# Performance work log

Hardware: AMD Instinct MI355X
Metric: run time of the kernel (lower is better)

The kernel has to match this reference:

```python
import jax, jax.numpy as jnp
import numpy as np

DEPTH = 512      # hidden width of each Linear (arg name 'depth' in the torch code)
WIDTH = 8        # number of hidden blocks (arg name 'width')
IN_DIM = 4       # x_dim=3 + is_unsteady=1
OUT_DIM = 4
N = 32768


def _mlp(x, W0, b0, Wh, bh, Wf, bf):
    # Faithful to torch Sequential: Linear, then (width-1) x [Linear, Tanh], then Linear.
    # Note: NO tanh after the very first Linear (matches the original module).
    h = x @ W0 + b0                      # [N, DEPTH]
    for i in range(Wh.shape[0]):         # width-1 hidden blocks (small fixed loop)
        h = jnp.tanh(h @ Wh[i] + bh[i])
    return h @ Wf + bf                   # [N, 4]


def setup_inputs() -> dict:
    key = jax.random.key(0)
    ks = jax.random.split(key, 8)
    s_in = 1.0 / np.sqrt(IN_DIM)
    s_h = 1.0 / np.sqrt(DEPTH)
    return {
        "x": jax.random.normal(ks[0], (N, IN_DIM), dtype=jnp.float32),
        "W0": jax.random.uniform(ks[1], (IN_DIM, DEPTH), jnp.float32, -s_in, s_in),
        "b0": jax.random.uniform(ks[2], (DEPTH,), jnp.float32, -s_in, s_in),
        "Wh": jax.random.uniform(ks[3], (WIDTH - 1, DEPTH, DEPTH), jnp.float32, -s_h, s_h),
        "bh": jax.random.uniform(ks[4], (WIDTH - 1, DEPTH), jnp.float32, -s_h, s_h),
        "Wf": jax.random.uniform(ks[5], (DEPTH, OUT_DIM), jnp.float32, -s_h, s_h),
        "bf": jax.random.uniform(ks[6], (OUT_DIM,), jnp.float32, -s_h, s_h),
    }


def reference(x, W0, b0, Wh, bh, Wf, bf):
    # a = MLP(x); then 4 batched VJPs w.r.t. x with cotangents e_0..e_3
    # (exactly what the torch curl() does with autograd.grad).
    a, vjp = jax.vjp(lambda xx: _mlp(xx, W0, b0, Wh, bh, Wf, bf), x)
    e = jnp.eye(OUT_DIM, dtype=a.dtype)
    da0 = vjp(jnp.broadcast_to(e[0], a.shape))[0]   # [N, 4] = d a_0 / d x
    da1 = vjp(jnp.broadcast_to(e[1], a.shape))[0]
    da2 = vjp(jnp.broadcast_to(e[2], a.shape))[0]
    dp  = vjp(jnp.broadcast_to(e[3], a.shape))[0]
    u = jnp.stack([
        da2[:, 1] - da1[:, 2],
        da0[:, 2] - da2[:, 0],
        da1[:, 0] - da0[:, 1],
        dp[:, 0], dp[:, 1], dp[:, 2],
    ], axis=1)                                       # [N, 6]
    return u
```

## Files before the change

kernel.cpp:

```cpp
#include <hip/hip_runtime.h>
#include <stdint.h>

typedef short bf16x8 __attribute__((ext_vector_type(8)));
typedef float f32x4  __attribute__((ext_vector_type(4)));
typedef uint32_t u32;

#define NSAMP  32768
#define D      512
#define RPB    16
#define NLAYER 7
#define KSN    16
#define WL_U32 131072

union U4B { uint4 u; u32 w[4]; bf16x8 s; };
__device__ __forceinline__ bf16x8 as_frag(uint4 v) { U4B c; c.u = v; return c.s; }

__device__ __forceinline__ u32 bfr(float f) {
    u32 b = __float_as_uint(f);
    return (b + 0x7fffu + ((b >> 16) & 1u)) >> 16;
}
__device__ __forceinline__ float bf2f(u32 h) { return __uint_as_float(h << 16); }
__device__ __forceinline__ u32 packpair(float v) {
    u32 h = bfr(v);
    u32 l = bfr(v - bf2f(h));
    return h | (l << 16);
}
__device__ __forceinline__ float fast_tanh(float z) {
    const float e = __expf(2.f * z);
    return 1.f - 2.f / (e + 1.f);
}

__global__ void pack_weights(const float* __restrict__ Wh,
                             u32* __restrict__ whi, u32* __restrict__ wlo) {
    const int L    = blockIdx.x >> 4;
    const int ks   = blockIdx.x & 15;
    const int lane = threadIdx.x & 63;
    const int half = threadIdx.x >> 6;
    const float* src = Wh + (size_t)L * D * D + (size_t)(ks * 32 + half * 8) * D;
    for (int nb = 0; nb < D; nb += 64) {
        const int n = nb + lane;
        float v[8];
        #pragma unroll
        for (int i = 0; i < 8; ++i) v[i] = src[(size_t)i * D + n];
        u32 hi[4], lo[4];
        #pragma unroll
        for (int j = 0; j < 4; ++j) {
            u32 h0 = bfr(v[2*j]),   l0 = bfr(v[2*j]   - bf2f(h0));
            u32 h1 = bfr(v[2*j+1]), l1 = bfr(v[2*j+1] - bf2f(h1));
            hi[j] = h0 | (h1 << 16);
            lo[j] = l0 | (l1 << 16);
        }
        const size_t idx4 = (size_t)((L * 16 + ks) * 512 + n) * 4 + half;
        *(uint4*)(whi + idx4 * 4) = *(uint4*)hi;
        *(uint4*)(wlo + idx4 * 4) = *(uint4*)lo;
    }
}

__global__ __launch_bounds__(1024)
void mlp_curl_mfma(const float* __restrict__ x,
                   const float* __restrict__ W0,
                   const float* __restrict__ b0,
                   const float* __restrict__ bhid,
                   const float* __restrict__ Wf,
                   const u32* __restrict__ whi,
                   const u32* __restrict__ wlo,
                   float* __restrict__ out)
{
    __shared__ uint4 AHi[4096];
    __shared__ uint4 ALo[1024];

    const int t    = threadIdx.x;
    const int g    = t >> 6, lane = t & 63;
    const int lrow = lane & 15, lq = lane >> 4;
    const int cg   = g;
    const int n0   = blockIdx.x * RPB;

    {
        const int R  = g >> 2, c4 = g & 3;
        const float4 xv = *(const float4*)(x + (size_t)(n0 + lrow) * 4);
        #pragma unroll
        for (int ksl = 0; ksl < 4; ++ksl) {
            const int ks = c4 * 4 + ksl;
            const int c0 = ks * 32 + lq * 8;
            float v[8];
            if (R == 0) {
                #pragma unroll
                for (int j = 0; j < 8; ++j)
                    v[j] = b0[c0 + j]
                         + xv.x * W0[c0 + j]         + xv.y * W0[D + c0 + j]
                         + xv.z * W0[2 * D + c0 + j] + xv.w * W0[3 * D + c0 + j];
                u32 pp[8];
                #pragma unroll
                for (int j = 0; j < 8; ++j) pp[j] = packpair(v[j]);
                uint4 hi, lo;
                hi.x = (pp[0] & 0xffffu) | (pp[1] << 16);  lo.x = (pp[0] >> 16) | (pp[1] & 0xffff0000u);
                hi.y = (pp[2] & 0xffffu) | (pp[3] << 16);  lo.y = (pp[2] >> 16) | (pp[3] & 0xffff0000u);
                hi.z = (pp[4] & 0xffffu) | (pp[5] << 16);  lo.z = (pp[4] >> 16) | (pp[5] & 0xffff0000u);
                hi.w = (pp[6] & 0xffffu) | (pp[7] << 16);  lo.w = (pp[6] >> 16) | (pp[7] & 0xffff0000u);
                AHi[ks * 64 + lane] = hi;
                ALo[ks * 64 + lane] = lo;
            } else {
                const float* wr = W0 + (size_t)(R - 1) * D;
                #pragma unroll
                for (int j = 0; j < 8; ++j) v[j] = wr[c0 + j];
                uint4 hi;
                hi.x = bfr(v[0]) | (bfr(v[1]) << 16);
                hi.y = bfr(v[2]) | (bfr(v[3]) << 16);
                hi.z = bfr(v[4]) | (bfr(v[5]) << 16);
                hi.w = bfr(v[6]) | (bfr(v[7]) << 16);
                AHi[(R * 16 + ks) * 64 + lane] = hi;
            }
        }
    }
    __syncthreads();

    const u32 boff0 = ((u32)(cg * 32 + lrow) * 4 + lq) * 4;
    const u32 boff1 = boff0 + 256;

    for (int L = 0; L < NLAYER; ++L) {
        const u32* __restrict__ whiL = whi + (size_t)L * WL_U32;
        const u32* __restrict__ wloL = wlo + (size_t)L * WL_U32;
        f32x4 acc[4][2];
        #pragma unroll
        for (int R = 0; R < 4; ++R) { acc[R][0] = (f32x4)0.f; acc[R][1] = (f32x4)0.f; }

        #pragma unroll 2
        for (int ks = 0; ks < KSN; ++ks) {
            const size_t off = (size_t)ks * 8192;
            const uint4 Bh0 = *(const uint4*)(whiL + off + boff0);
            const uint4 Bh1 = *(const uint4*)(whiL + off + boff1);
            const uint4 Bl0 = *(const uint4*)(wloL + off + boff0);
            const uint4 Bl1 = *(const uint4*)(wloL + off + boff1);
            {
                const bf16x8 a_hi = as_frag(AHi[ks * 64 + lane]);
                const bf16x8 a_lo = as_frag(ALo[ks * 64 + lane]);
                const bf16x8 b0h = as_frag(Bh0), b0l = as_frag(Bl0);
                const bf16x8 b1h = as_frag(Bh1), b1l = as_frag(Bl1);
                acc[0][0] = __builtin_amdgcn_mfma_f32_16x16x32_bf16(a_lo, b0h, acc[0][0], 0, 0, 0);
                acc[0][0] = __builtin_amdgcn_mfma_f32_16x16x32_bf16(a_hi, b0l, acc[0][0], 0, 0, 0);
                acc[0][0] = __builtin_amdgcn_mfma_f32_16x16x32_bf16(a_hi, b0h, acc[0][0], 0, 0, 0);
                acc[0][1] = __builtin_amdgcn_mfma_f32_16x16x32_bf16(a_lo, b1h, acc[0][1], 0, 0, 0);
                acc[0][1] = __builtin_amdgcn_mfma_f32_16x16x32_bf16(a_hi, b1l, acc[0][1], 0, 0, 0);
                acc[0][1] = __builtin_amdgcn_mfma_f32_16x16x32_bf16(a_hi, b1h, acc[0][1], 0, 0, 0);
            }
            #pragma unroll
            for (int R = 1; R < 4; ++R) {
                const bf16x8 a_hi = as_frag(AHi[(R * 16 + ks) * 64 + lane]);
                const bf16x8 b0h = as_frag(Bh0), b0l = as_frag(Bl0);
                const bf16x8 b1h = as_frag(Bh1), b1l = as_frag(Bl1);
                acc[R][0] = __builtin_amdgcn_mfma_f32_16x16x32_bf16(a_hi, b0l, acc[R][0], 0, 0, 0);
                acc[R][0] = __builtin_amdgcn_mfma_f32_16x16x32_bf16(a_hi, b0h, acc[R][0], 0, 0, 0);
                acc[R][1] = __builtin_amdgcn_mfma_f32_16x16x32_bf16(a_hi, b1l, acc[R][1], 0, 0, 0);
                acc[R][1] = __builtin_amdgcn_mfma_f32_16x16x32_bf16(a_hi, b1h, acc[R][1], 0, 0, 0);
            }
        }
        __syncthreads();

        float tp[2][4];
        #pragma unroll
        for (int ct = 0; ct < 2; ++ct) {
            const int col = cg * 32 + ct * 16 + lrow;
            const float bias = bhid[(size_t)L * D + col];
            const int k = ct * 16 + lrow;
            #pragma unroll
            for (int q = 0; q < 4; ++q) {
                const float h = fast_tanh(acc[0][ct][q] + bias);
                tp[ct][q] = (1.f - h) * (1.f + h);
                if (L < NLAYER - 1) {
                    const u32 pp = packpair(h);
                    const u32 byte = ((u32)((cg * 64) + (k >> 3) * 16 + (lq * 4 + q)) << 4)
                                   | ((u32)(k & 7) << 1);
                    *(uint16_t*)((char*)AHi + byte) = (uint16_t)(pp & 0xffffu);
                    *(uint16_t*)((char*)ALo + byte) = (uint16_t)(pp >> 16);
                }
            }
        }

        if (L < NLAYER - 1) {
            #pragma unroll
            for (int R = 1; R < 4; ++R)
                #pragma unroll
                for (int ct = 0; ct < 2; ++ct) {
                    const int k = ct * 16 + lrow;
                    #pragma unroll
                    for (int q = 0; q < 4; ++q) {
                        const u32 hb = bfr(acc[R][ct][q] * tp[ct][q]);
                        const u32 byte = ((u32)(((R * 16 + cg) * 64) + (k >> 3) * 16 + (lq * 4 + q)) << 4)
                                       | ((u32)(k & 7) << 1);
                        *(uint16_t*)((char*)AHi + byte) = (uint16_t)hb;
                    }
                }
        } else {
            #pragma unroll
            for (int i = 0; i < 3; ++i) {
                float Jrow[4][4];
                #pragma unroll
                for (int q = 0; q < 4; ++q)
                    #pragma unroll
                    for (int o = 0; o < 4; ++o) Jrow[q][o] = 0.f;
                #pragma unroll
                for (int ct = 0; ct < 2; ++ct) {
                    const int col = cg * 32 + ct * 16 + lrow;
                    const float4 wf = *(const float4*)(Wf + (size_t)col * 4);
                    #pragma unroll
                    for (int q = 0; q < 4; ++q) {
                        const float jv = acc[i + 1][ct][q] * tp[ct][q];
                        Jrow[q][0] += jv * wf.x;
                        Jrow[q][1] += jv * wf.y;
                        Jrow[q][2] += jv * wf.z;
                        Jrow[q][3] += jv * wf.w;
                    }
                }
                #pragma unroll
                for (int m = 1; m <= 8; m <<= 1)
                    #pragma unroll
                    for (int q = 0; q < 4; ++q)
                        #pragma unroll
                        for (int o = 0; o < 4; ++o)
                            Jrow[q][o] += __shfl_xor(Jrow[q][o], m);
                if (lrow == 0) {
                    float* JT = (float*)AHi;
                    #pragma unroll
                    for (int q = 0; q < 4; ++q) {
                        const int s = lq * 4 + q;
                        #pragma unroll
                        for (int o = 0; o < 4; ++o)
                            JT[((cg * 3 + i) * 16 + s) * 4 + o] = Jrow[q][o];
                    }
                }
            }
        }
        __syncthreads();
    }

    if (t < RPB * 6) {
        const float* JT = (const float*)AHi;
        const int s = t / 6, c = t % 6;
        float J[3][4];
        #pragma unroll
        for (int i = 0; i < 3; ++i)
            #pragma unroll
            for (int o = 0; o < 4; ++o) {
                float v = 0.f;
                for (int w = 0; w < 16; ++w) v += JT[((w * 3 + i) * 16 + s) * 4 + o];
                J[i][o] = v;
            }
        float v;
        if      (c == 0) v = J[1][2] - J[2][1];
        else if (c == 1) v = J[2][0] - J[0][2];
        else if (c == 2) v = J[0][1] - J[1][0];
        else if (c == 3) v = J[0][3];
        else if (c == 4) v = J[1][3];
        else             v = J[2][3];
        out[(size_t)(n0 + s) * 6 + c] = v;
    }
}

extern "C" void kernel_launch(void* const* d_in, const int* in_sizes, int n_in,
                              void* d_out, int out_size, void* d_ws, size_t ws_size,
                              hipStream_t stream) {
    const float* x  = (const float*)d_in[0];
    const float* W0 = (const float*)d_in[1];
    const float* b0 = (const float*)d_in[2];
    const float* Wh = (const float*)d_in[3];
    const float* bh = (const float*)d_in[4];
    const float* Wf = (const float*)d_in[5];
    u32* whi = (u32*)d_ws;
    u32* wlo = whi + (size_t)NLAYER * WL_U32;
    pack_weights<<<NLAYER * 16, 256, 0, stream>>>(Wh, whi, wlo);
    mlp_curl_mfma<<<NSAMP / RPB, 1024, 0, stream>>>(x, W0, b0, bh, Wf, whi, wlo, (float*)d_out);
}
```

Measured before the change: 1.112 ms.

## Pack primal and tangent rows into two MFMA tiles with eight samples per block

Each block now handles 8 samples instead of 16. The forward activations and the three tangent streams are packed into two 16-row MFMA tiles: rows 0-7 of the first tile hold the primal and rows 8-15 hold the first tangent. Each of 8 warps covers 64 output columns, and the block size is halved to 512 threads with a launch-bounds occupancy hint, so shared memory per block shrinks. The aim is better occupancy and fewer wasted tangent tiles. In exchange, each sample re-reads more weight data from L2, and the hi/lo split-precision MFMA is now also applied to the first tangent rows, which adds MFMA work.

```diff
diff --git a/kernel.cpp b/kernel.cpp
--- a/kernel.cpp
+++ b/kernel.cpp
@@ -7,7 +7,7 @@
 
 #define NSAMP  32768
 #define D      512
-#define RPB    16
+#define RPB    8
 #define NLAYER 7
 #define KSN    16
 #define WL_U32 131072
@@ -56,7 +56,7 @@
     }
 }
 
-__global__ __launch_bounds__(1024)
+__global__ __launch_bounds__(512, 4)
 void mlp_curl_mfma(const float* __restrict__ x,
                    const float* __restrict__ W0,
                    const float* __restrict__ b0,
@@ -66,149 +66,131 @@
                    const u32* __restrict__ wlo,
                    float* __restrict__ out)
 {
-    __shared__ uint4 AHi[4096];
+    __shared__ uint4 AHi[2048];
     __shared__ uint4 ALo[1024];
+    __shared__ float JT[768];
 
     const int t    = threadIdx.x;
     const int g    = t >> 6, lane = t & 63;
     const int lrow = lane & 15, lq = lane >> 4;
-    const int cg   = g;
+    const int c0   = g * 64;
     const int n0   = blockIdx.x * RPB;
 
     {
-        const int R  = g >> 2, c4 = g & 3;
-        const float4 xv = *(const float4*)(x + (size_t)(n0 + lrow) * 4);
-        #pragma unroll
-        for (int ksl = 0; ksl < 4; ++ksl) {
-            const int ks = c4 * 4 + ksl;
-            const int c0 = ks * 32 + lq * 8;
-            float v[8];
-            if (R == 0) {
-                #pragma unroll
-                for (int j = 0; j < 8; ++j)
-                    v[j] = b0[c0 + j]
-                         + xv.x * W0[c0 + j]         + xv.y * W0[D + c0 + j]
-                         + xv.z * W0[2 * D + c0 + j] + xv.w * W0[3 * D + c0 + j];
-                u32 pp[8];
-                #pragma unroll
-                for (int j = 0; j < 8; ++j) pp[j] = packpair(v[j]);
-                uint4 hi, lo;
-                hi.x = (pp[0] & 0xffffu) | (pp[1] << 16);  lo.x = (pp[0] >> 16) | (pp[1] & 0xffff0000u);
-                hi.y = (pp[2] & 0xffffu) | (pp[3] << 16);  lo.y = (pp[2] >> 16) | (pp[3] & 0xffff0000u);
-                hi.z = (pp[4] & 0xffffu) | (pp[5] << 16);  lo.z = (pp[4] >> 16) | (pp[5] & 0xffff0000u);
-                hi.w = (pp[6] & 0xffffu) | (pp[7] << 16);  lo.w = (pp[6] >> 16) | (pp[7] & 0xffff0000u);
-                AHi[ks * 64 + lane] = hi;
-                ALo[ks * 64 + lane] = lo;
-            } else {
-                const float* wr = W0 + (size_t)(R - 1) * D;
-                #pragma unroll
-                for (int j = 0; j < 8; ++j) v[j] = wr[c0 + j];
-                uint4 hi;
-                hi.x = bfr(v[0]) | (bfr(v[1]) << 16);
-                hi.y = bfr(v[2]) | (bfr(v[3]) << 16);
-                hi.z = bfr(v[4]) | (bfr(v[5]) << 16);
-                hi.w = bfr(v[6]) | (bfr(v[7]) << 16);
-                AHi[(R * 16 + ks) * 64 + lane] = hi;
-            }
+        const int r = lrow;
+        const float4 xv = *(const float4*)(x + (size_t)(n0 + (r & 7)) * 4);
+        #pragma unroll
+        for (int ksl = 0; ksl < 2; ++ksl) {
+            const int ks = g * 2 + ksl;
+            const int cb = ks * 32 + lq * 8;
+            float v0[8], v1[8];
+            #pragma unroll
+            for (int j = 0; j < 8; ++j) {
+                const int c = cb + j;
+                const float w0 = W0[c], w1 = W0[D + c], w2 = W0[2*D + c], w3 = W0[3*D + c];
+                v0[j] = (r < 8) ? (b0[c] + xv.x*w0 + xv.y*w1 + xv.z*w2 + xv.w*w3) : w0;
+                v1[j] = (r < 8) ? w1 : w2;
+            }
+            u32 pp[8];
+            #pragma unroll
+            for (int j = 0; j < 8; ++j) pp[j] = packpair(v0[j]);
+            uint4 hi, lo;
+            hi.x = (pp[0] & 0xffffu) | (pp[1] << 16);  lo.x = (pp[0] >> 16) | (pp[1] & 0xffff0000u);
+            hi.y = (pp[2] & 0xffffu) | (pp[3] << 16);  lo.y = (pp[2] >> 16) | (pp[3] & 0xffff0000u);
+            hi.z = (pp[4] & 0xffffu) | (pp[5] << 16);  lo.z = (pp[4] >> 16) | (pp[5] & 0xffff0000u);
+            hi.w = (pp[6] & 0xffffu) | (pp[7] << 16);  lo.w = (pp[6] >> 16) | (pp[7] & 0xffff0000u);
+            AHi[ks * 64 + lane] = hi;
+            ALo[ks * 64 + lane] = lo;
+            uint4 h1;
+            h1.x = bfr(v1[0]) | (bfr(v1[1]) << 16);
+            h1.y = bfr(v1[2]) | (bfr(v1[3]) << 16);
+            h1.z = bfr(v1[4]) | (bfr(v1[5]) << 16);
+            h1.w = bfr(v1[6]) | (bfr(v1[7]) << 16);
+            AHi[(16 + ks) * 64 + lane] = h1;
         }
     }
     __syncthreads();
 
-    const u32 boff0 = ((u32)(cg * 32 + lrow) * 4 + lq) * 4;
-    const u32 boff1 = boff0 + 256;
+    u32 boff[4];
+    #pragma unroll
+    for (int ct = 0; ct < 4; ++ct)
+        boff[ct] = ((u32)(c0 + ct * 16 + lrow) * 4 + (u32)lq) * 4;
 
     for (int L = 0; L < NLAYER; ++L) {
         const u32* __restrict__ whiL = whi + (size_t)L * WL_U32;
         const u32* __restrict__ wloL = wlo + (size_t)L * WL_U32;
-        f32x4 acc[4][2];
-        #pragma unroll
-        for (int R = 0; R < 4; ++R) { acc[R][0] = (f32x4)0.f; acc[R][1] = (f32x4)0.f; }
+        f32x4 acc[2][4];
+        #pragma unroll
+        for (int ct = 0; ct < 4; ++ct) { acc[0][ct] = (f32x4)0.f; acc[1][ct] = (f32x4)0.f; }
 
         #pragma unroll 2
         for (int ks = 0; ks < KSN; ++ks) {
+            const bf16x8 a0h = as_frag(AHi[ks * 64 + lane]);
+            const bf16x8 a0l = as_frag(ALo[ks * 64 + lane]);
+            const bf16x8 a1h = as_frag(AHi[(16 + ks) * 64 + lane]);
             const size_t off = (size_t)ks * 8192;
-            const uint4 Bh0 = *(const uint4*)(whiL + off + boff0);
-            const uint4 Bh1 = *(const uint4*)(whiL + off + boff1);
-            const uint4 Bl0 = *(const uint4*)(wloL + off + boff0);
-            const uint4 Bl1 = *(const uint4*)(wloL + off + boff1);
-            {
-                const bf16x8 a_hi = as_frag(AHi[ks * 64 + lane]);
-                const bf16x8 a_lo = as_frag(ALo[ks * 64 + lane]);
-                const bf16x8 b0h = as_frag(Bh0), b0l = as_frag(Bl0);
-                const bf16x8 b1h = as_frag(Bh1), b1l = as_frag(Bl1);
-                acc[0][0] = __builtin_amdgcn_mfma_f32_16x16x32_bf16(a_lo, b0h, acc[0][0], 0, 0, 0);
-                acc[0][0] = __builtin_amdgcn_mfma_f32_16x16x32_bf16(a_hi, b0l, acc[0][0], 0, 0, 0);
-                acc[0][0] = __builtin_amdgcn_mfma_f32_16x16x32_bf16(a_hi, b0h, acc[0][0], 0, 0, 0);
-                acc[0][1] = __builtin_amdgcn_mfma_f32_16x16x32_bf16(a_lo, b1h, acc[0][1], 0, 0, 0);
-                acc[0][1] = __builtin_amdgcn_mfma_f32_16x16x32_bf16(a_hi, b1l, acc[0][1], 0, 0, 0);
-                acc[0][1] = __builtin_amdgcn_mfma_f32_16x16x32_bf16(a_hi, b1h, acc[0][1], 0, 0, 0);
-            }
-            #pragma unroll
-            for (int R = 1; R < 4; ++R) {
-                const bf16x8 a_hi = as_frag(AHi[(R * 16 + ks) * 64 + lane]);
-                const bf16x8 b0h = as_frag(Bh0), b0l = as_frag(Bl0);
-                const bf16x8 b1h = as_frag(Bh1), b1l = as_frag(Bl1);
-                acc[R][0] = __builtin_amdgcn_mfma_f32_16x16x32_bf16(a_hi, b0l, acc[R][0], 0, 0, 0);
-                acc[R][0] = __builtin_amdgcn_mfma_f32_16x16x32_bf16(a_hi, b0h, acc[R][0], 0, 0, 0);
-                acc[R][1] = __builtin_amdgcn_mfma_f32_16x16x32_bf16(a_hi, b1l, acc[R][1], 0, 0, 0);
-                acc[R][1] = __builtin_amdgcn_mfma_f32_16x16x32_bf16(a_hi, b1h, acc[R][1], 0, 0, 0);
+            #pragma unroll
+            for (int ct = 0; ct < 4; ++ct) {
+                const bf16x8 bh = as_frag(*(const uint4*)(whiL + off + boff[ct]));
+                const bf16x8 bl = as_frag(*(const uint4*)(wloL + off + boff[ct]));
+                acc[0][ct] = __builtin_amdgcn_mfma_f32_16x16x32_bf16(a0l, bh, acc[0][ct], 0, 0, 0);
+                acc[0][ct] = __builtin_amdgcn_mfma_f32_16x16x32_bf16(a0h, bl, acc[0][ct], 0, 0, 0);
+                acc[0][ct] = __builtin_amdgcn_mfma_f32_16x16x32_bf16(a0h, bh, acc[0][ct], 0, 0, 0);
+                acc[1][ct] = __builtin_amdgcn_mfma_f32_16x16x32_bf16(a1h, bl, acc[1][ct], 0, 0, 0);
+                acc[1][ct] = __builtin_amdgcn_mfma_f32_16x16x32_bf16(a1h, bh, acc[1][ct], 0, 0, 0);
             }
         }
         __syncthreads();
 
-        float tp[2][4];
-        #pragma unroll
-        for (int ct = 0; ct < 2; ++ct) {
-            const int col = cg * 32 + ct * 16 + lrow;
+        float tpv[4][4];
+        #pragma unroll
+        for (int ct = 0; ct < 4; ++ct) {
+            const int col  = c0 + ct * 16 + lrow;
             const float bias = bhid[(size_t)L * D + col];
-            const int k = ct * 16 + lrow;
+            const int ks_s = g * 2 + (ct >> 1);
+            const int k_in = (ct & 1) * 16 + lrow;
             #pragma unroll
             for (int q = 0; q < 4; ++q) {
-                const float h = fast_tanh(acc[0][ct][q] + bias);
-                tp[ct][q] = (1.f - h) * (1.f + h);
+                const float z0 = acc[0][ct][q];
+                const float h  = fast_tanh(z0 + bias);
+                const float tv = __shfl((1.f - h) * (1.f + h), lane & 31);
+                tpv[ct][q] = tv;
                 if (L < NLAYER - 1) {
-                    const u32 pp = packpair(h);
-                    const u32 byte = ((u32)((cg * 64) + (k >> 3) * 16 + (lq * 4 + q)) << 4)
-                                   | ((u32)(k & 7) << 1);
-                    *(uint16_t*)((char*)AHi + byte) = (uint16_t)(pp & 0xffffu);
-                    *(uint16_t*)((char*)ALo + byte) = (uint16_t)(pp >> 16);
+                    const float v0 = (lane < 32) ? h : z0 * tv;
+                    const u32 pp = packpair(v0);
+                    const u32 fl = (u32)(((k_in >> 3) * 16) + lq * 4 + q);
+                    const u32 b0b = ((u32)(ks_s * 64) + fl) * 16 + ((u32)(k_in & 7) << 1);
+                    *(uint16_t*)((char*)AHi + b0b) = (uint16_t)(pp & 0xffffu);
+                    *(uint16_t*)((char*)ALo + b0b) = (uint16_t)(pp >> 16);
+                    const float v1 = acc[1][ct][q] * tv;
+                    const u32 b1b = ((u32)((16 + ks_s) * 64) + fl) * 16 + ((u32)(k_in & 7) << 1);
+                    *(uint16_t*)((char*)AHi + b1b) = (uint16_t)bfr(v1);
                 }
             }
         }
 
-        if (L < NLAYER - 1) {
-            #pragma unroll
-            for (int R = 1; R < 4; ++R)
-                #pragma unroll
-                for (int ct = 0; ct < 2; ++ct) {
-                    const int k = ct * 16 + lrow;
-                    #pragma unroll
-                    for (int q = 0; q < 4; ++q) {
-                        const u32 hb = bfr(acc[R][ct][q] * tp[ct][q]);
-                        const u32 byte = ((u32)(((R * 16 + cg) * 64) + (k >> 3) * 16 + (lq * 4 + q)) << 4)
-                                       | ((u32)(k & 7) << 1);
-                        *(uint16_t*)((char*)AHi + byte) = (uint16_t)hb;
-                    }
-                }
-        } else {
+        if (L == NLAYER - 1) {
             #pragma unroll
             for (int i = 0; i < 3; ++i) {
-                float Jrow[4][4];
+                float Jr[4][4];
                 #pragma unroll
                 for (int q = 0; q < 4; ++q)
                     #pragma unroll
-                    for (int o = 0; o < 4; ++o) Jrow[q][o] = 0.f;
+                    for (int o = 0; o < 4; ++o) Jr[q][o] = 0.f;
                 #pragma unroll
-                for (int ct = 0; ct < 2; ++ct) {
-                    const int col = cg * 32 + ct * 16 + lrow;
+                for (int ct = 0; ct < 4; ++ct) {
+                    const int col = c0 + ct * 16 + lrow;
                     const float4 wf = *(const float4*)(Wf + (size_t)col * 4);
                     #pragma unroll
                     for (int q = 0; q < 4; ++q) {
-                        const float jv = acc[i + 1][ct][q] * tp[ct][q];
-                        Jrow[q][0] += jv * wf.x;
-                        Jrow[q][1] += jv * wf.y;
-                        Jrow[q][2] += jv * wf.z;
-                        Jrow[q][3] += jv * wf.w;
+                        float jv;
+                        if (i == 0)      jv = (lane >= 32) ? acc[0][ct][q] * tpv[ct][q] : 0.f;
+                        else if (i == 1) jv = (lane <  32) ? acc[1][ct][q] * tpv[ct][q] : 0.f;
+                        else             jv = (lane >= 32) ? acc[1][ct][q] * tpv[ct][q] : 0.f;
+                        Jr[q][0] += jv * wf.x;
+                        Jr[q][1] += jv * wf.y;
+                        Jr[q][2] += jv * wf.z;
+                        Jr[q][3] += jv * wf.w;
                     }
                 }
                 #pragma unroll
@@ -217,15 +199,14 @@
                     for (int q = 0; q < 4; ++q)
                         #pragma unroll
                         for (int o = 0; o < 4; ++o)
-                            Jrow[q][o] += __shfl_xor(Jrow[q][o], m);
-                if (lrow == 0) {
-                    float* JT = (float*)AHi;
+                            Jr[q][o] += __shfl_xor(Jr[q][o], m);
+                const bool wr = (i == 1) ? (lq < 2) : (lq >= 2);
+                if (lrow == 0 && wr) {
                     #pragma unroll
                     for (int q = 0; q < 4; ++q) {
-                        const int s = lq * 4 + q;
-                        #pragma unroll
-                        for (int o = 0; o < 4; ++o)
-                            JT[((cg * 3 + i) * 16 + s) * 4 + o] = Jrow[q][o];
+                        const int s = (lq & 1) * 4 + q;
+                        *(float4*)&JT[((g * 3 + i) * 8 + s) * 4] =
+                            make_float4(Jr[q][0], Jr[q][1], Jr[q][2], Jr[q][3]);
                     }
                 }
             }
@@ -234,7 +215,6 @@
     }
 
     if (t < RPB * 6) {
-        const float* JT = (const float*)AHi;
         const int s = t / 6, c = t % 6;
         float J[3][4];
         #pragma unroll
@@ -242,7 +222,7 @@
             #pragma unroll
             for (int o = 0; o < 4; ++o) {
                 float v = 0.f;
-                for (int w = 0; w < 16; ++w) v += JT[((w * 3 + i) * 16 + s) * 4 + o];
+                for (int w = 0; w < 8; ++w) v += JT[((w * 3 + i) * 8 + s) * 4 + o];
                 J[i][o] = v;
             }
         float v;
@@ -268,5 +248,5 @@
     u32* whi = (u32*)d_ws;
     u32* wlo = whi + (size_t)NLAYER * WL_U32;
     pack_weights<<<NLAYER * 16, 256, 0, stream>>>(Wh, whi, wlo);
-    mlp_curl_mfma<<<NSAMP / RPB, 1024, 0, stream>>>(x, W0, b0, bh, Wf, whi, wlo, (float*)d_out);
-}
+    mlp_curl_mfma<<<NSAMP / RPB, 512, 0, stream>>>(x, W0, b0, bh, Wf, whi, wlo, (float*)d_out);
+}
```

Measured after the change: 1.839 ms. 1.65x slower.
